# Kernel tuning notes

Hardware: AMD Instinct MI355X
Metric: run time of the kernel (lower is better)

## Reference

```python
import jax, jax.numpy as jnp
import numpy as np

DELTA = 1e-3  # inverse-distance kernel smoothing from NEC paper
NUM_NEIGHBOURS = 50


def setup_inputs() -> dict:
    key = jax.random.key(0)
    k1, k2, k3 = jax.random.split(key, 3)
    B, C, D = 1024, 500000, 64
    return {
        "keys": jax.random.normal(k1, (B, D), dtype=jnp.float32),
        "table_keys": jax.random.normal(k2, (C, D), dtype=jnp.float32),
        "table_values": jax.random.normal(k3, (C,), dtype=jnp.float32),
    }


def reference(keys, table_keys, table_values):
    # Brute-force kNN search: squared L2 distances [B, C]
    d2 = (
        jnp.sum(keys * keys, axis=1, keepdims=True)
        - 2.0 * (keys @ table_keys.T)
        + jnp.sum(table_keys * table_keys, axis=1)[None, :]
    )
    _, idx = jax.lax.top_k(-d2, NUM_NEIGHBOURS)  # [B, K] smallest distances

    neighbours = table_keys[idx]  # [B, K, D] gather
    # recompute exact squared distances against gathered neighbours
    sq = jnp.sum((keys[:, None, :] - neighbours) ** 2, axis=2)  # [B, K]
    w = 1.0 / (sq + DELTA)
    w = w / jnp.sum(w, axis=1, keepdims=True)
    v = table_values[idx]  # [B, K]
    return jnp.sum(w * v, axis=1)  # [B]
```

## Files before the change

kernel.cpp:

```cpp
#include <hip/hip_runtime.h>
#include <math.h>


#define DELTA_SMOOTH 1e-3f
#define K_NEIGH 50
#define MAXCAP 8192
#define NBINS 256
#define MARGIN_T 1.5f
#define MARGIN_Q 26
#define RPB 1024
#define QTILE 512
#define SDEPTH 6
#define LW 768
#define CVL 2048
#define S_SAMP 16384
#define T_SAMP 13
#define FSAMPLE 2048
#define FTARGET 6
#define FMARGIN 0.75f
#define FQB 4

typedef __attribute__((ext_vector_type(8))) short short8;
typedef __attribute__((ext_vector_type(4))) float f32x4;
typedef __attribute__((address_space(1))) const unsigned int g_u32;
typedef __attribute__((address_space(3))) unsigned int l_u32;

__device__ __forceinline__ unsigned f2bf(float f) {
  unsigned u = __float_as_uint(f);
  return ((u + 0x7fffu + ((u >> 16) & 1u)) >> 16) & 0xffffu;
}

__global__ __launch_bounds__(256) void convert_kernel(
    const float* __restrict__ tk, uint4* __restrict__ tkbf,
    float* __restrict__ tnh2, int C, int padded) {
  int t = blockIdx.x * 256 + threadIdx.x;
  int r = t >> 3;
  if (r >= padded) return;
  int c = t & 7;
  int rs = r < C ? r : C - 1;
  const float4* src = (const float4*)(tk + (size_t)rs * 64 + c * 8);
  float4 a = src[0], b = src[1];
  float sq = a.x * a.x + a.y * a.y + a.z * a.z + a.w * a.w
           + b.x * b.x + b.y * b.y + b.z * b.z + b.w * b.w;
  sq += __shfl_xor(sq, 1); sq += __shfl_xor(sq, 2); sq += __shfl_xor(sq, 4);
  if (c == 0) tnh2[r] = sq * 0.5f;
  uint4 u;
  u.x = f2bf(a.x) | (f2bf(a.y) << 16);
  u.y = f2bf(a.z) | (f2bf(a.w) << 16);
  u.z = f2bf(b.x) | (f2bf(b.y) << 16);
  u.w = f2bf(b.z) | (f2bf(b.w) << 16);
  tkbf[(size_t)(r >> 6) * 512 + (r & 63) * 8 + (c ^ (r & 7))] = u;
}

__global__ __launch_bounds__(512, 4) void qthresh_mfma(
    const uint4* __restrict__ tkbf, const float* __restrict__ keys,
    const float* __restrict__ tnh2, unsigned short* __restrict__ dsamp) {
  __shared__ __align__(16) uint4 bstage[2][512];
  __shared__ float tnh_lds[128];
  int tid = threadIdx.x;
  int qt = blockIdx.x & 1;
  int chunk = blockIdx.x >> 1;
  int qbase = qt * QTILE;
  int rstart = chunk * 128;
  if (tid < 128) tnh_lds[tid] = tnh2[rstart + tid];
  int lane = tid & 63, wq = tid >> 6, l15 = lane & 15, quad = lane >> 4;
  short8 afrag[4][2];
  #pragma unroll
  for (int mt = 0; mt < 4; ++mt) {
    const float* kp = keys + (size_t)(qbase + wq * 64 + mt * 16 + l15) * 64 + quad * 8;
    #pragma unroll
    for (int s = 0; s < 2; ++s) {
      float4 x = *(const float4*)(kp + s * 32);
      float4 y = *(const float4*)(kp + s * 32 + 4);
      short8 a;
      a[0] = (short)f2bf(x.x); a[1] = (short)f2bf(x.y);
      a[2] = (short)f2bf(x.z); a[3] = (short)f2bf(x.w);
      a[4] = (short)f2bf(y.x); a[5] = (short)f2bf(y.y);
      a[6] = (short)f2bf(y.z); a[7] = (short)f2bf(y.w);
      afrag[mt][s] = a;
    }
  }
  const uint4* gbase = tkbf + (size_t)(rstart >> 6) * 512;
  __builtin_amdgcn_global_load_lds((g_u32*)(gbase + tid),
                                   (l_u32*)(&bstage[0][wq * 64]), 16, 0, 0);
  __syncthreads();
  f32x4 zero4 = {0.f, 0.f, 0.f, 0.f};
  for (int it = 0; it < 2; ++it) {
    if (it == 0)
      __builtin_amdgcn_global_load_lds((g_u32*)(gbase + 512 + tid),
                                       (l_u32*)(&bstage[1][wq * 64]), 16, 0, 0);
    const unsigned char* buf = (const unsigned char*)bstage[it & 1];
    #pragma unroll
    for (int half = 0; half < 2; ++half) {
      short8 b[2][2];
      #pragma unroll
      for (int tt = 0; tt < 2; ++tt) {
        int nloc = half * 32 + tt * 16 + l15;
        #pragma unroll
        for (int s = 0; s < 2; ++s) {
          int c = s * 4 + quad;
          unsigned addr = (unsigned)(nloc * 128 + ((c ^ (nloc & 7)) << 4));
          b[tt][s] = *(const short8*)(buf + addr);
        }
      }
      f32x4 acc[4][2];
      #pragma unroll
      for (int mt = 0; mt < 4; ++mt)
        #pragma unroll
        for (int tt = 0; tt < 2; ++tt) {
          f32x4 a0 = __builtin_amdgcn_mfma_f32_16x16x32_bf16(afrag[mt][0], b[tt][0], zero4, 0, 0, 0);
          acc[mt][tt] = __builtin_amdgcn_mfma_f32_16x16x32_bf16(afrag[mt][1], b[tt][1], a0, 0, 0, 0);
        }
      #pragma unroll
      for (int tt = 0; tt < 2; ++tt) {
        int rloc = it * 64 + half * 32 + tt * 16 + l15;
        float tnh = tnh_lds[rloc];
        int n = rstart + rloc;
        #pragma unroll
        for (int mt = 0; mt < 4; ++mt) {
          #pragma unroll
          for (int r = 0; r < 4; ++r) {
            int ql = wq * 64 + mt * 16 + quad * 4 + r;
            int u = (int)fmaf(tnh - acc[mt][tt][r], 512.f, 32768.f);
            u = u < 0 ? 0 : (u > 65535 ? 65535 : u);
            dsamp[(size_t)(qbase + ql) * S_SAMP + n] = (unsigned short)u;
          }
        }
      }
    }
    __syncthreads();
  }
}

__global__ __launch_bounds__(256) void qthresh_scan(
    const unsigned short* __restrict__ dsamp, float* __restrict__ thrh,
    int* __restrict__ cnt) {
  int q = blockIdx.x;
  __shared__ unsigned hist[512];
  int tid = threadIdx.x;
  hist[tid] = 0u; hist[tid + 256] = 0u;
  __syncthreads();
  const unsigned short* dp = dsamp + (size_t)q * S_SAMP;
  for (int i = tid; i < S_SAMP; i += 256) atomicAdd(&hist[dp[i] >> 7], 1u);
  __syncthreads();
  if (tid == 0) {
    unsigned cum = 0; int bstar = 511;
    for (int b = 0; b < 512; ++b) {
      cum += hist[b];
      if (cum >= (unsigned)T_SAMP) { bstar = b; break; }
    }
    float thr = (float)(bstar + 1) * 0.5f - 128.f + MARGIN_T;
    thrh[q] = 0.5f * thr;
    cnt[q] = 0;
  }
}

__global__ __launch_bounds__(512, 4) void filter_mfma_fast(
    const uint4* __restrict__ tkbf, const float* __restrict__ keys,
    const float* __restrict__ tnh2, const float* __restrict__ thrh,
    int* __restrict__ cnt, unsigned* __restrict__ candi, int C, int cap) {
  __shared__ __align__(16) uint4 bstage[4][512];
  __shared__ float tnh_lds[RPB];
  __shared__ float thr_lds[QTILE];
  __shared__ unsigned scnt[QTILE];
  __shared__ unsigned sbuf[QTILE * SDEPTH];

  int tid = threadIdx.x;
  int qt = blockIdx.x & 1;
  int chunk = blockIdx.x >> 1;
  int qbase = qt * QTILE;
  int rstart = chunk * RPB;

  tnh_lds[tid] = tnh2[rstart + tid];
  tnh_lds[tid + 512] = tnh2[rstart + tid + 512];
  thr_lds[tid] = thrh[qbase + tid];
  scnt[tid] = 0u;

  int lane = tid & 63, wq = tid >> 6, l15 = lane & 15, quad = lane >> 4;

  short8 afrag[4][2];
  #pragma unroll
  for (int mt = 0; mt < 4; ++mt) {
    const float* kp = keys + (size_t)(qbase + wq * 64 + mt * 16 + l15) * 64 + quad * 8;
    #pragma unroll
    for (int s = 0; s < 2; ++s) {
      float4 x = *(const float4*)(kp + s * 32);
      float4 y = *(const float4*)(kp + s * 32 + 4);
      short8 a;
      a[0] = (short)f2bf(x.x); a[1] = (short)f2bf(x.y);
      a[2] = (short)f2bf(x.z); a[3] = (short)f2bf(x.w);
      a[4] = (short)f2bf(y.x); a[5] = (short)f2bf(y.y);
      a[6] = (short)f2bf(y.z); a[7] = (short)f2bf(y.w);
      afrag[mt][s] = a;
    }
  }

  __syncthreads();

  const uint4* gbase = tkbf + (size_t)(rstart >> 6) * 512;
  const int ITERS = RPB / 64;
  #pragma unroll
  for (int s = 0; s < 3; ++s)
    __builtin_amdgcn_global_load_lds((g_u32*)(gbase + (size_t)s * 512 + tid),
                                     (l_u32*)(&bstage[s][wq * 64]), 16, 0, 0);

  float hmax[4];
  #pragma unroll
  for (int mt = 0; mt < 4; ++mt) {
    float h0 = thr_lds[wq * 64 + mt * 16 + quad * 4 + 0];
    float h1 = thr_lds[wq * 64 + mt * 16 + quad * 4 + 1];
    float h2 = thr_lds[wq * 64 + mt * 16 + quad * 4 + 2];
    float h3 = thr_lds[wq * 64 + mt * 16 + quad * 4 + 3];
    hmax[mt] = fmaxf(fmaxf(h0, h1), fmaxf(h2, h3));
  }

  f32x4 zero4 = {0.f, 0.f, 0.f, 0.f};

  for (int it = 0; it < ITERS; ++it) {
    if (it < ITERS - 2) {
      asm volatile("s_waitcnt vmcnt(2)\n\ts_barrier" ::: "memory");
    } else if (it == ITERS - 2) {
      asm volatile("s_waitcnt vmcnt(1)\n\ts_barrier" ::: "memory");
    } else {
      asm volatile("s_waitcnt vmcnt(0)\n\ts_barrier" ::: "memory");
    }
    __builtin_amdgcn_sched_barrier(0);
    if (it + 3 < ITERS) {
      __builtin_amdgcn_global_load_lds((g_u32*)(gbase + (size_t)(it + 3) * 512 + tid),
                                       (l_u32*)(&bstage[(it + 3) & 3][wq * 64]), 16, 0, 0);
    }
    const unsigned char* buf = (const unsigned char*)bstage[it & 3];
    #pragma unroll
    for (int half = 0; half < 2; ++half) {
      short8 b[2][2];
      #pragma unroll
      for (int tt = 0; tt < 2; ++tt) {
        int nloc = half * 32 + tt * 16 + l15;
        #pragma unroll
        for (int s = 0; s < 2; ++s) {
          int c = s * 4 + quad;
          unsigned addr = (unsigned)(nloc * 128 + ((c ^ (nloc & 7)) << 4));
          b[tt][s] = *(const short8*)(buf + addr);
        }
      }
      f32x4 acc[4][2];
      #pragma unroll
      for (int mt = 0; mt < 4; ++mt)
        #pragma unroll
        for (int tt = 0; tt < 2; ++tt) {
          f32x4 a0 = __builtin_amdgcn_mfma_f32_16x16x32_bf16(afrag[mt][0], b[tt][0], zero4, 0, 0, 0);
          acc[mt][tt] = __builtin_amdgcn_mfma_f32_16x16x32_bf16(afrag[mt][1], b[tt][1], a0, 0, 0, 0);
        }
      #pragma unroll
      for (int tt = 0; tt < 2; ++tt) {
        int rloc = it * 64 + half * 32 + tt * 16 + l15;
        float tnh = tnh_lds[rloc];
        int n = rstart + rloc;
        #pragma unroll
        for (int mt = 0; mt < 4; ++mt) {
          float mx4 = fmaxf(fmaxf(acc[mt][tt][0], acc[mt][tt][1]),
                            fmaxf(acc[mt][tt][2], acc[mt][tt][3]));
          if (__builtin_expect(mx4 + hmax[mt] > tnh, 0)) {
            #pragma unroll
            for (int r = 0; r < 4; ++r) {
              int ql = wq * 64 + mt * 16 + quad * 4 + r;
              float t = tnh - acc[mt][tt][r];
              if (t < thr_lds[ql] && n < C) {
                int d2q = (int)fmaf(t, 32.f, 2048.f);
                d2q = d2q < 0 ? 0 : (d2q > 8191 ? 8191 : d2q);
                unsigned v = ((unsigned)d2q << 19) | (unsigned)n;
                unsigned p = atomicAdd(&scnt[ql], 1u);
                if (p < SDEPTH) {
                  sbuf[ql * SDEPTH + p] = v;
                } else {
                  int g = atomicAdd(&cnt[qbase + ql], 1);
                  if (g < cap) candi[(size_t)(qbase + ql) * cap + g] = v;
                }
              }
            }
          }
        }
      }
    }
  }
  __syncthreads();
  int m = (int)scnt[tid];
  if (m > SDEPTH) m = SDEPTH;
  if (m > 0) {
    int base = atomicAdd(&cnt[qbase + tid], m);
    for (int j = 0; j < m; ++j) {
      int g = base + j;
      if (g < cap) candi[(size_t)(qbase + tid) * cap + g] = sbuf[tid * SDEPTH + j];
    }
  }
}

__global__ __launch_bounds__(256) void qthresh_fb(
    const float* __restrict__ keys, const float* __restrict__ tk,
    float* __restrict__ thr, float* __restrict__ qnorm, int C) {
  int q0 = blockIdx.x * FQB;
  __shared__ __align__(16) float kq[FQB * 64];
  __shared__ unsigned hist[FQB][NBINS];
  __shared__ float qn4[FQB];
  int tid = threadIdx.x;
  for (int i = tid; i < FQB * 64; i += 256) kq[i] = keys[(size_t)q0 * 64 + i];
  for (int i = tid; i < FQB * NBINS; i += 256) (&hist[0][0])[i] = 0u;
  __syncthreads();
  if (tid < FQB) {
    float s = 0.f;
    for (int j = 0; j < 64; ++j) { float v = kq[tid * 64 + j]; s += v * v; }
    qn4[tid] = s;
  }
  __syncthreads();
  int kc = tid & 3;
  const float4* kq4 = (const float4*)kq;
  float4 kf[FQB][4];
  #pragma unroll
  for (int jq = 0; jq < FQB; ++jq)
    #pragma unroll
    for (int u = 0; u < 4; ++u) kf[jq][u] = kq4[jq * 16 + kc * 4 + u];
  int S = FSAMPLE < C ? FSAMPLE : C;
  for (int r = tid >> 2; r < S; r += 64) {
    const float4* trow = (const float4*)(tk + (size_t)r * 64 + kc * 16);
    float4 t0 = trow[0], t1 = trow[1], t2 = trow[2], t3 = trow[3];
    float tn = t0.x * t0.x + t0.y * t0.y + t0.z * t0.z + t0.w * t0.w
             + t1.x * t1.x + t1.y * t1.y + t1.z * t1.z + t1.w * t1.w
             + t2.x * t2.x + t2.y * t2.y + t2.z * t2.z + t2.w * t2.w
             + t3.x * t3.x + t3.y * t3.y + t3.z * t3.z + t3.w * t3.w;
    tn += __shfl_xor(tn, 1); tn += __shfl_xor(tn, 2);
    float dot[FQB];
    #pragma unroll
    for (int jq = 0; jq < FQB; ++jq) {
      float s = kf[jq][0].x * t0.x + kf[jq][0].y * t0.y + kf[jq][0].z * t0.z + kf[jq][0].w * t0.w
              + kf[jq][1].x * t1.x + kf[jq][1].y * t1.y + kf[jq][1].z * t1.z + kf[jq][1].w * t1.w
              + kf[jq][2].x * t2.x + kf[jq][2].y * t2.y + kf[jq][2].z * t2.z + kf[jq][2].w * t2.w
              + kf[jq][3].x * t3.x + kf[jq][3].y * t3.y + kf[jq][3].z * t3.z + kf[jq][3].w * t3.w;
      s += __shfl_xor(s, 1); s += __shfl_xor(s, 2);
      dot[jq] = s;
    }
    if (kc == 0) {
      #pragma unroll
      for (int jq = 0; jq < FQB; ++jq) {
        float d2 = qn4[jq] + tn - 2.f * dot[jq];
        int b = (int)d2;
        b = b < 0 ? 0 : (b > NBINS - 1 ? NBINS - 1 : b);
        atomicAdd(&hist[jq][b], 1u);
      }
    }
  }
  __syncthreads();
  if (tid < FQB) {
    unsigned cum = 0; int bstar = NBINS - 1;
    for (int b = 0; b < NBINS; ++b) {
      cum += hist[tid][b];
      if (cum >= (unsigned)FTARGET) { bstar = b; break; }
    }
    thr[q0 + tid] = (float)(bstar + 1) + FMARGIN - qn4[tid];
    qnorm[q0 + tid] = qn4[tid];
  }
}

__global__ __launch_bounds__(512, 4) void filter_fb(
    const float* __restrict__ keys, const float* __restrict__ tk,
    const float* __restrict__ thr, const float* __restrict__ qnorm,
    int* __restrict__ cnt, unsigned* __restrict__ candi, int C, int cap) {
  __shared__ float tnstage[64];
  __shared__ float thr_lds[QTILE];
  __shared__ float qn_lds[QTILE];
  __shared__ unsigned scnt[QTILE];
  __shared__ unsigned sbuf[QTILE * SDEPTH];
  __shared__ __align__(16) unsigned char bstage[64 * 128];
  int tid = threadIdx.x;
  int qt = blockIdx.x & 1;
  int chunk = blockIdx.x >> 1;
  int qbase = qt * QTILE;
  int rstart = chunk * RPB;
  thr_lds[tid] = thr[qbase + tid];
  qn_lds[tid] = qnorm[qbase + tid];
  scnt[tid] = 0u;
  int lane = tid & 63, wq = tid >> 6, l15 = lane & 15, quad = lane >> 4;
  short8 afrag[4][2];
  #pragma unroll
  for (int mt = 0; mt < 4; ++mt) {
    const float* kp = keys + (size_t)(qbase + wq * 64 + mt * 16 + l15) * 64 + quad * 8;
    #pragma unroll
    for (int s = 0; s < 2; ++s) {
      float4 x = *(const float4*)(kp + s * 32);
      float4 y = *(const float4*)(kp + s * 32 + 4);
      short8 a;
      a[0] = (short)f2bf(x.x); a[1] = (short)f2bf(x.y);
      a[2] = (short)f2bf(x.z); a[3] = (short)f2bf(x.w);
      a[4] = (short)f2bf(y.x); a[5] = (short)f2bf(y.y);
      a[6] = (short)f2bf(y.z); a[7] = (short)f2bf(y.w);
      afrag[mt][s] = a;
    }
  }
  __syncthreads();
  float hq[4];
  #pragma unroll
  for (int mt = 0; mt < 4; ++mt) {
    float h0 = thr_lds[wq * 64 + mt * 16 + quad * 4 + 0];
    float h1 = thr_lds[wq * 64 + mt * 16 + quad * 4 + 1];
    float h2 = thr_lds[wq * 64 + mt * 16 + quad * 4 + 2];
    float h3 = thr_lds[wq * 64 + mt * 16 + quad * 4 + 3];
    hq[mt] = fmaxf(fmaxf(h0, h1), fmaxf(h2, h3));
  }
  int srow = tid >> 3, scol = tid & 7;
  unsigned sbyte = (unsigned)(srow * 128 + ((scol ^ (srow & 7)) << 4));
  const int ITERS = RPB / 64;
  int r0 = rstart + srow; if (r0 > C - 1) r0 = C - 1;
  float4 pa = *(const float4*)(tk + (size_t)r0 * 64 + scol * 8);
  float4 pb = *(const float4*)(tk + (size_t)r0 * 64 + scol * 8 + 4);
  f32x4 zero4 = {0.f, 0.f, 0.f, 0.f};
  for (int it = 0; it < ITERS; ++it) {
    float part = pa.x * pa.x + pa.y * pa.y + pa.z * pa.z + pa.w * pa.w
               + pb.x * pb.x + pb.y * pb.y + pb.z * pb.z + pb.w * pb.w;
    part += __shfl_xor(part, 1); part += __shfl_xor(part, 2); part += __shfl_xor(part, 4);
    if ((tid & 7) == 0) tnstage[srow] = part;
    uint4 u;
    u.x = f2bf(pa.x) | (f2bf(pa.y) << 16);
    u.y = f2bf(pa.z) | (f2bf(pa.w) << 16);
    u.z = f2bf(pb.x) | (f2bf(pb.y) << 16);
    u.w = f2bf(pb.z) | (f2bf(pb.w) << 16);
    *(uint4*)(bstage + sbyte) = u;
    __syncthreads();
    if (it + 1 < ITERS) {
      int rn = rstart + (it + 1) * 64 + srow; if (rn > C - 1) rn = C - 1;
      pa = *(const float4*)(tk + (size_t)rn * 64 + scol * 8);
      pb = *(const float4*)(tk + (size_t)rn * 64 + scol * 8 + 4);
    }
    #pragma unroll
    for (int half = 0; half < 2; ++half) {
      short8 b[2][2];
      #pragma unroll
      for (int tt = 0; tt < 2; ++tt) {
        int nloc = half * 32 + tt * 16 + l15;
        #pragma unroll
        for (int s = 0; s < 2; ++s) {
          int c = s * 4 + quad;
          unsigned addr = (unsigned)(nloc * 128 + ((c ^ (nloc & 7)) << 4));
          b[tt][s] = *(const short8*)(bstage + addr);
        }
      }
      f32x4 acc[4][2];
      #pragma unroll
      for (int mt = 0; mt < 4; ++mt)
        #pragma unroll
        for (int tt = 0; tt < 2; ++tt) {
          f32x4 a0 = __builtin_amdgcn_mfma_f32_16x16x32_bf16(afrag[mt][0], b[tt][0], zero4, 0, 0, 0);
          acc[mt][tt] = __builtin_amdgcn_mfma_f32_16x16x32_bf16(afrag[mt][1], b[tt][1], a0, 0, 0, 0);
        }
      #pragma unroll
      for (int tt = 0; tt < 2; ++tt) {
        float tn = tnstage[half * 32 + tt * 16 + l15];
        int n = rstart + it * 64 + half * 32 + tt * 16 + l15;
        #pragma unroll
        for (int mt = 0; mt < 4; ++mt) {
          float d0 = fmaf(-2.f, acc[mt][tt][0], tn);
          float d1 = fmaf(-2.f, acc[mt][tt][1], tn);
          float d2 = fmaf(-2.f, acc[mt][tt][2], tn);
          float d3 = fmaf(-2.f, acc[mt][tt][3], tn);
          float mn4 = fminf(fminf(d0, d1), fminf(d2, d3));
          if (mn4 < hq[mt]) {
            float dd[4] = {d0, d1, d2, d3};
            #pragma unroll
            for (int r = 0; r < 4; ++r) {
              int ql = wq * 64 + mt * 16 + quad * 4 + r;
              if (dd[r] < thr_lds[ql] && n < C) {
                float d2f = dd[r] + qn_lds[ql];
                int d2q = (int)(d2f * 16.f);
                d2q = d2q < 0 ? 0 : (d2q > 8191 ? 8191 : d2q);
                unsigned v = ((unsigned)d2q << 19) | (unsigned)n;
                unsigned p = atomicAdd(&scnt[ql], 1u);
                if (p < SDEPTH) sbuf[ql * SDEPTH + p] = v;
                else {
                  int g = atomicAdd(&cnt[qbase + ql], 1);
                  if (g < cap) candi[(size_t)(qbase + ql) * cap + g] = v;
                }
              }
            }
          }
        }
      }
    }
    __syncthreads();
  }
  int m = (int)scnt[tid];
  if (m > SDEPTH) m = SDEPTH;
  if (m > 0) {
    int base = atomicAdd(&cnt[qbase + tid], m);
    for (int j = 0; j < m; ++j) {
      int g = base + j;
      if (g < cap) candi[(size_t)(qbase + tid) * cap + g] = sbuf[tid * SDEPTH + j];
    }
  }
}

__global__ __launch_bounds__(256) void select_kernel(
    const float* __restrict__ keys, const float* __restrict__ tk,
    const float* __restrict__ tv, const int* __restrict__ cnt,
    const unsigned* __restrict__ candi, float* __restrict__ out, int cap) {
  int q = blockIdx.x;
  __shared__ unsigned cvl[CVL];
  __shared__ unsigned hist[NBINS];
  __shared__ unsigned wsum[4];
  __shared__ unsigned minq_sh;
  __shared__ int b50_sh;
  __shared__ int lidx[LW];
  __shared__ unsigned ed2[LW];
  __shared__ int m_sh;
  __shared__ float redw[4], redwv[4];
  int tid = threadIdx.x;
  int lane = tid & 63;
  int wid = tid >> 6;
  int n = cnt[q];
  if (n > cap) n = cap;
  hist[tid] = 0u;
  if (tid == 0) { minq_sh = 0xffffffffu; b50_sh = NBINS - 1; m_sh = 0; }
  __syncthreads();
  const unsigned* cv = candi + (size_t)q * cap;
  unsigned mn = 0xffffffffu;
  for (int i = tid; i < n; i += 256) {
    unsigned v = cv[i];
    if (i < CVL) cvl[i] = v;
    unsigned d = v >> 19; if (d < mn) mn = d;
  }
  #pragma unroll
  for (int off = 1; off < 64; off <<= 1) { unsigned o = __shfl_xor(mn, off); if (o < mn) mn = o; }
  if (lane == 0) atomicMin(&minq_sh, mn);
  __syncthreads();
  unsigned base = minq_sh;
  for (int i = tid; i < n; i += 256) {
    unsigned v = (i < CVL) ? cvl[i] : cv[i];
    unsigned d = (v >> 19) - base;
    unsigned b = d >> 1; if (b > NBINS - 1) b = NBINS - 1;
    atomicAdd(&hist[b], 1u);
  }
  __syncthreads();
  unsigned h = hist[tid];
  unsigned p = h;
  #pragma unroll
  for (int off = 1; off < 64; off <<= 1) {
    unsigned v = __shfl_up(p, off);
    if (lane >= off) p += v;
  }
  if (lane == 63) wsum[wid] = p;
  __syncthreads();
  unsigned add = 0;
  for (int w2 = 0; w2 < wid; ++w2) add += wsum[w2];
  p += add;
  if (p >= (unsigned)K_NEIGH && p - h < (unsigned)K_NEIGH) b50_sh = tid;
  __syncthreads();
  unsigned Tq = base + (((unsigned)(b50_sh + 1)) << 1) + MARGIN_Q;
  for (int i = tid; i < n; i += 256) {
    unsigned v = (i < CVL) ? cvl[i] : cv[i];
    if ((v >> 19) <= Tq) {
      int p2 = atomicAdd(&m_sh, 1);
      if (p2 < LW) lidx[p2] = (int)(v & 0x7ffffu);
    }
  }
  __syncthreads();
  int m = m_sh; if (m > LW) m = LW;
  float kqv = keys[(size_t)q * 64 + lane];
  for (int i0 = wid * 4; i0 < m; i0 += 16) {
    int mm = m - i0; if (mm > 4) mm = 4;
    int idx[4]; float t[4];
    for (int u = 0; u < mm; ++u) idx[u] = lidx[i0 + u];
    for (int u = 0; u < mm; ++u) t[u] = tk[(size_t)idx[u] * 64 + lane];
    for (int u = 0; u < mm; ++u) {
      float d = t[u] - kqv;
      float s = d * d;
      #pragma unroll
      for (int off = 1; off < 64; off <<= 1) s += __shfl_xor(s, off);
      if (lane == 0) ed2[i0 + u] = __float_as_uint(s);
    }
  }
  __syncthreads();
  float accw = 0.f, accwv = 0.f;
  for (int i = tid; i < m; i += 256) {
    unsigned long long key = ((unsigned long long)ed2[i] << 19) | (unsigned)lidx[i];
    int rank = 0;
    for (int j = 0; j < m; ++j) {
      unsigned long long kj = ((unsigned long long)ed2[j] << 19) | (unsigned)lidx[j];
      rank += (kj < key) ? 1 : 0;
    }
    if (rank < K_NEIGH) {
      float d2 = __uint_as_float(ed2[i]);
      float w = 1.f / (d2 + DELTA_SMOOTH);
      accw += w;
      accwv += w * tv[lidx[i]];
    }
  }
  #pragma unroll
  for (int off = 1; off < 64; off <<= 1) {
    accw += __shfl_xor(accw, off);
    accwv += __shfl_xor(accwv, off);
  }
  if (lane == 0) { redw[wid] = accw; redwv[wid] = accwv; }
  __syncthreads();
  if (tid == 0) {
    float sw = redw[0] + redw[1] + redw[2] + redw[3];
    float swv = redwv[0] + redwv[1] + redwv[2] + redwv[3];
    out[q] = swv / sw;
  }
}

extern "C" void kernel_launch(void* const* d_in, const int* in_sizes, int n_in,
                              void* d_out, int out_size, void* d_ws, size_t ws_size,
                              hipStream_t stream) {
  const float* keys = (const float*)d_in[0];
  const float* tk   = (const float*)d_in[1];
  const float* tv   = (const float*)d_in[2];
  float* out = (float*)d_out;
  int B = in_sizes[0] / 64;
  int C = in_sizes[2];

  int nchunks = (C + RPB - 1) / RPB;
  int padded = nchunks * RPB;

  char* w = (char*)d_ws;
  float* thrh = (float*)w;  w += (size_t)B * 4;
  float* qnfb = (float*)w;  w += (size_t)B * 4;
  int*   cnt  = (int*)w;    w += (size_t)B * 4;
  size_t fixed = (size_t)(w - (char*)d_ws);

  size_t tk_bytes = (size_t)padded * 128 + (size_t)padded * 4;
  size_t dsamp_bytes = (size_t)S_SAMP * (size_t)B * 2;
  size_t region = ws_size > fixed + tk_bytes ? ws_size - fixed - tk_bytes : 0;
  bool fast = region >= dsamp_bytes && region >= 2048ull * (size_t)B * 4;

  if (fast) {
    uint4* tkbf = (uint4*)w;              w += (size_t)padded * 128;
    float* tnh2 = (float*)w;              w += (size_t)padded * 4;
    unsigned short* dsamp = (unsigned short*)w;
    unsigned* candi = (unsigned*)w;
    int cap = (int)(region / (4ull * (size_t)B));
    if (cap > MAXCAP) cap = MAXCAP;
    convert_kernel<<<(padded * 8 + 255) / 256, 256, 0, stream>>>(tk, tkbf, tnh2, C, padded);
    qthresh_mfma<<<256, 512, 0, stream>>>(tkbf, keys, tnh2, dsamp);
    qthresh_scan<<<B, 256, 0, stream>>>(dsamp, thrh, cnt);
    filter_mfma_fast<<<nchunks * 2, 512, 0, stream>>>(tkbf, keys, tnh2, thrh,
                                                      cnt, candi, C, cap);
    select_kernel<<<B, 256, 0, stream>>>(keys, tk, tv, cnt, candi, out, cap);
  } else {
    unsigned* candi = (unsigned*)w;
    int cap = (int)((ws_size - fixed) / (4ull * (size_t)B));
    if (cap > MAXCAP) cap = MAXCAP;
    if (cap < 1) cap = 1;
    hipMemsetAsync(cnt, 0, (size_t)B * 4, stream);
    qthresh_fb<<<B / FQB, 256, 0, stream>>>(keys, tk, thrh, qnfb, C);
    filter_fb<<<nchunks * 2, 512, 0, stream>>>(keys, tk, thrh, qnfb,
                                               cnt, candi, C, cap);
    select_kernel<<<B, 256, 0, stream>>>(keys, tk, tv, cnt, candi, out, cap);
  }
}
```

Measured before the change: 443.8 us.

## Process two staged tiles per barrier phase and keep thresholds in registers

The main scan loop now handles two 64-row tiles per barrier phase, issuing two global-to-LDS prefetches per phase. This halves the number of workgroup barriers in the loop. Per-query thresholds are loaded once into registers instead of being read from LDS for every candidate check. The coarse max-based filter is dropped for a direct per-element test. Padded rows now get a huge norm so the n<C check can be removed. The trade-offs are more register pressure and a shallower effective prefetch distance.

```diff
diff --git a/kernel.cpp b/kernel.cpp
--- a/kernel.cpp
+++ b/kernel.cpp
@@ -43,7 +43,7 @@
   float sq = a.x * a.x + a.y * a.y + a.z * a.z + a.w * a.w
            + b.x * b.x + b.y * b.y + b.z * b.z + b.w * b.w;
   sq += __shfl_xor(sq, 1); sq += __shfl_xor(sq, 2); sq += __shfl_xor(sq, 4);
-  if (c == 0) tnh2[r] = sq * 0.5f;
+  if (c == 0) tnh2[r] = (r < C) ? sq * 0.5f : 3e38f;
   uint4 u;
   u.x = f2bf(a.x) | (f2bf(a.y) << 16);
   u.y = f2bf(a.z) | (f2bf(a.w) << 16);
@@ -197,75 +197,72 @@
 
   __syncthreads();
 
+  float thrr[4][4];
+  #pragma unroll
+  for (int mt = 0; mt < 4; ++mt)
+    #pragma unroll
+    for (int r = 0; r < 4; ++r)
+      thrr[mt][r] = thr_lds[wq * 64 + mt * 16 + quad * 4 + r];
+
   const uint4* gbase = tkbf + (size_t)(rstart >> 6) * 512;
-  const int ITERS = RPB / 64;
-  #pragma unroll
-  for (int s = 0; s < 3; ++s)
+  const int PHASES = RPB / 128;
+  #pragma unroll
+  for (int s = 0; s < 2; ++s)
     __builtin_amdgcn_global_load_lds((g_u32*)(gbase + (size_t)s * 512 + tid),
                                      (l_u32*)(&bstage[s][wq * 64]), 16, 0, 0);
 
-  float hmax[4];
-  #pragma unroll
-  for (int mt = 0; mt < 4; ++mt) {
-    float h0 = thr_lds[wq * 64 + mt * 16 + quad * 4 + 0];
-    float h1 = thr_lds[wq * 64 + mt * 16 + quad * 4 + 1];
-    float h2 = thr_lds[wq * 64 + mt * 16 + quad * 4 + 2];
-    float h3 = thr_lds[wq * 64 + mt * 16 + quad * 4 + 3];
-    hmax[mt] = fmaxf(fmaxf(h0, h1), fmaxf(h2, h3));
-  }
-
   f32x4 zero4 = {0.f, 0.f, 0.f, 0.f};
 
-  for (int it = 0; it < ITERS; ++it) {
-    if (it < ITERS - 2) {
-      asm volatile("s_waitcnt vmcnt(2)\n\ts_barrier" ::: "memory");
-    } else if (it == ITERS - 2) {
-      asm volatile("s_waitcnt vmcnt(1)\n\ts_barrier" ::: "memory");
+  for (int ph = 0; ph < PHASES; ++ph) {
+    __builtin_amdgcn_s_barrier();
+    if (ph + 1 < PHASES) {
+      #pragma unroll
+      for (int s = 0; s < 2; ++s)
+        __builtin_amdgcn_global_load_lds(
+            (g_u32*)(gbase + ((size_t)(ph + 1) * 2 + s) * 512 + tid),
+            (l_u32*)(&bstage[(((ph + 1) * 2 + s)) & 3][wq * 64]), 16, 0, 0);
+      asm volatile("s_waitcnt vmcnt(2)" ::: "memory");
     } else {
-      asm volatile("s_waitcnt vmcnt(0)\n\ts_barrier" ::: "memory");
+      asm volatile("s_waitcnt vmcnt(0)" ::: "memory");
     }
     __builtin_amdgcn_sched_barrier(0);
-    if (it + 3 < ITERS) {
-      __builtin_amdgcn_global_load_lds((g_u32*)(gbase + (size_t)(it + 3) * 512 + tid),
-                                       (l_u32*)(&bstage[(it + 3) & 3][wq * 64]), 16, 0, 0);
-    }
-    const unsigned char* buf = (const unsigned char*)bstage[it & 3];
-    #pragma unroll
-    for (int half = 0; half < 2; ++half) {
-      short8 b[2][2];
-      #pragma unroll
-      for (int tt = 0; tt < 2; ++tt) {
-        int nloc = half * 32 + tt * 16 + l15;
-        #pragma unroll
-        for (int s = 0; s < 2; ++s) {
-          int c = s * 4 + quad;
-          unsigned addr = (unsigned)(nloc * 128 + ((c ^ (nloc & 7)) << 4));
-          b[tt][s] = *(const short8*)(buf + addr);
-        }
-      }
-      f32x4 acc[4][2];
-      #pragma unroll
-      for (int mt = 0; mt < 4; ++mt)
+    #pragma unroll
+    for (int sl = 0; sl < 2; ++sl) {
+      const unsigned char* buf = (const unsigned char*)bstage[(ph * 2 + sl) & 3];
+      int itrow = ph * 128 + sl * 64;
+      #pragma unroll
+      for (int half = 0; half < 2; ++half) {
+        short8 b[2][2];
         #pragma unroll
         for (int tt = 0; tt < 2; ++tt) {
-          f32x4 a0 = __builtin_amdgcn_mfma_f32_16x16x32_bf16(afrag[mt][0], b[tt][0], zero4, 0, 0, 0);
-          acc[mt][tt] = __builtin_amdgcn_mfma_f32_16x16x32_bf16(afrag[mt][1], b[tt][1], a0, 0, 0, 0);
-        }
-      #pragma unroll
-      for (int tt = 0; tt < 2; ++tt) {
-        int rloc = it * 64 + half * 32 + tt * 16 + l15;
-        float tnh = tnh_lds[rloc];
-        int n = rstart + rloc;
-        #pragma unroll
-        for (int mt = 0; mt < 4; ++mt) {
-          float mx4 = fmaxf(fmaxf(acc[mt][tt][0], acc[mt][tt][1]),
-                            fmaxf(acc[mt][tt][2], acc[mt][tt][3]));
-          if (__builtin_expect(mx4 + hmax[mt] > tnh, 0)) {
+          int nloc = half * 32 + tt * 16 + l15;
+          #pragma unroll
+          for (int s = 0; s < 2; ++s) {
+            int c = s * 4 + quad;
+            unsigned addr = (unsigned)(nloc * 128 + ((c ^ (nloc & 7)) << 4));
+            b[tt][s] = *(const short8*)(buf + addr);
+          }
+        }
+        f32x4 acc[4][2];
+        #pragma unroll
+        for (int mt = 0; mt < 4; ++mt)
+          #pragma unroll
+          for (int tt = 0; tt < 2; ++tt) {
+            f32x4 a0 = __builtin_amdgcn_mfma_f32_16x16x32_bf16(afrag[mt][0], b[tt][0], zero4, 0, 0, 0);
+            acc[mt][tt] = __builtin_amdgcn_mfma_f32_16x16x32_bf16(afrag[mt][1], b[tt][1], a0, 0, 0, 0);
+          }
+        #pragma unroll
+        for (int tt = 0; tt < 2; ++tt) {
+          int rloc = itrow + half * 32 + tt * 16 + l15;
+          float tnh = tnh_lds[rloc];
+          int n = rstart + rloc;
+          #pragma unroll
+          for (int mt = 0; mt < 4; ++mt) {
             #pragma unroll
             for (int r = 0; r < 4; ++r) {
-              int ql = wq * 64 + mt * 16 + quad * 4 + r;
               float t = tnh - acc[mt][tt][r];
-              if (t < thr_lds[ql] && n < C) {
+              if (__builtin_expect(t < thrr[mt][r], 0)) {
+                int ql = wq * 64 + mt * 16 + quad * 4 + r;
                 int d2q = (int)fmaf(t, 32.f, 2048.f);
                 d2q = d2q < 0 ? 0 : (d2q > 8191 ? 8191 : d2q);
                 unsigned v = ((unsigned)d2q << 19) | (unsigned)n;
```

Result: faster. 379.0 us (-14.6%).
